# Performance work log

Measured on AMD Instinct MI355X. Metric: run time of the kernel, lower is better.

The kernel has to match this reference:

```python
import jax, jax.numpy as jnp
import numpy as np

NUM_THING = 80
THING_STUFF_IDS = np.concatenate([np.arange(80), np.arange(80, 133)])  # thing_class_ids + stuff_class_ids
H_OUT, W_OUT = 641, 641
PIXEL_CONF_THR = 0.4
CLASS_CONF_THR = 0.7
NEG = -1e9  # mask value standing in for removing undetected slots


def _resize_bilinear_align_corners(x, h_out, w_out):
    # x: [h_in, w_in, C]; tf.compat.v1.image.resize_bilinear(..., align_corners=True)
    h_in, w_in = x.shape[0], x.shape[1]
    ys = jnp.linspace(0.0, h_in - 1.0, h_out)
    xs = jnp.linspace(0.0, w_in - 1.0, w_out)
    y0 = jnp.floor(ys).astype(jnp.int32)
    x0 = jnp.floor(xs).astype(jnp.int32)
    y1 = jnp.minimum(y0 + 1, h_in - 1)
    x1 = jnp.minimum(x0 + 1, w_in - 1)
    wy = (ys - y0.astype(ys.dtype))[:, None, None]
    wx = (xs - x0.astype(xs.dtype))[None, :, None]
    rows = x[y0] * (1.0 - wy) + x[y1] * wy          # [h_out, w_in, C]
    return rows[:, x0] * (1.0 - wx) + rows[:, x1] * wx  # [h_out, w_out, C]


def setup_inputs() -> dict:
    key = jax.random.key(0)
    k1, k2 = jax.random.split(key)
    pixel_space_mask_logits = jax.random.normal(k1, (161, 161, 128), dtype=jnp.float32)
    transformer_class_probs = jax.random.uniform(k2, (128, 134), dtype=jnp.float32)
    return {"pixel_space_mask_logits": pixel_space_mask_logits,
            "transformer_class_probs": transformer_class_probs}


def reference(pixel_space_mask_logits, transformer_class_probs):
    # --- _get_transformer_class_prediction (void channel dropped first) ---
    probs = transformer_class_probs[:, :-1]                     # [M, C]
    cls_pred = jnp.argmax(probs, axis=-1).astype(jnp.float32)   # [M]
    cls_conf = jnp.max(probs, axis=-1)                          # [M]
    detected = cls_conf >= CLASS_CONF_THR                       # [M] bool
    num_detections = jnp.sum(detected.astype(jnp.int32))
    # index of each detected slot within the detected subset (matches tf.gather order)
    det_subset_index = jnp.cumsum(detected.astype(jnp.int32)) - 1  # [M]

    # --- resize logits to full image (pieces=1 -> single full-width piece) ---
    resized = _resize_bilinear_align_corners(pixel_space_mask_logits, H_OUT, W_OUT)  # [H, W, M]

    # mask out undetected slots instead of gathering (same math, static shape)
    masked = jnp.where(detected[None, None, :], resized, NEG)   # [H, W, M]

    full_max = jnp.max(resized, axis=-1)                        # [H, W]
    det_max = jnp.max(masked, axis=-1)                          # [H, W]
    detected_pixel = (full_max == det_max).astype(jnp.float32)

    pixel_conf = jnp.max(jax.nn.softmax(masked, axis=-1), axis=-1)
    confident_region = (pixel_conf > PIXEL_CONF_THR).astype(jnp.float32) * detected_pixel

    argmax_slot = jnp.argmax(masked, axis=-1)                   # [H, W] slot index
    mask_id_map = det_subset_index[argmax_slot]                 # index within detected subset
    sem_float = cls_pred[argmax_slot]                           # detected_mask_class_pred gathered

    thing_mask = (sem_float < NUM_THING).astype(jnp.float32) * confident_region
    stuff_mask = (sem_float >= NUM_THING).astype(jnp.float32) * confident_region
    semantic_map = jnp.asarray(THING_STUFF_IDS, jnp.int32)[jnp.round(sem_float).astype(jnp.int32)]
    mask_id_map_plus_one = mask_id_map.astype(jnp.int32) + 1

    # --- empty-detection branch (tf.cond) expressed as select ---
    has_det = num_detections > 0
    mask_id_map_plus_one = jnp.where(has_det, mask_id_map_plus_one, jnp.ones_like(mask_id_map_plus_one))
    semantic_map = jnp.where(has_det, semantic_map, jnp.zeros_like(semantic_map))
    thing_mask = jnp.where(has_det, thing_mask, jnp.zeros_like(thing_mask))
    stuff_mask = jnp.where(has_det, stuff_mask, jnp.zeros_like(stuff_mask))
    return (mask_id_map_plus_one, semantic_map, thing_mask, stuff_mask)
```

## Files before the change

### kernel.cpp

```cpp
#include <hip/hip_runtime.h>

#pragma clang fp contract(off)

#define NP 410881

__global__ __launch_bounds__(1024) void slot_kernel(
    const float* __restrict__ probs, float* __restrict__ cls_pred,
    int* __restrict__ det_idx, unsigned long long* __restrict__ det_mask,
    int* __restrict__ num_det) {
  __shared__ float s_val[128];
  __shared__ int s_arg[128];
  __shared__ int s_tot0;
  int tid = threadIdx.x;
  int wv = tid >> 6, lane = tid & 63;

  float bvv[8];
  int bii[8];
#pragma unroll
  for (int k = 0; k < 8; ++k) {
    int r = wv * 8 + k;
    const float* row = probs + r * 134;
    float v0 = row[lane];
    float v1 = row[lane + 64];
    float v2 = (lane < 5) ? row[lane + 128] : -1.0f;
    float bv = v0;
    int bi = lane;
    if (v1 > bv) { bv = v1; bi = lane + 64; }
    if (v2 > bv) { bv = v2; bi = lane + 128; }
    bvv[k] = bv; bii[k] = bi;
  }
#pragma unroll
  for (int k = 0; k < 8; ++k) {
    float bv = bvv[k];
    int bi = bii[k];
#pragma unroll
    for (int off = 32; off; off >>= 1) {
      float ov = __shfl_xor(bv, off);
      int oi = __shfl_xor(bi, off);
      if (ov > bv || (ov == bv && oi < bi)) { bv = ov; bi = oi; }
    }
    if (lane == 0) { s_val[wv * 8 + k] = bv; s_arg[wv * 8 + k] = bi; }
  }
  __syncthreads();

  bool flag = false;
  unsigned long long b = 0;
  if (tid < 128) flag = s_val[tid] >= 0.7f;
  if (wv < 2) b = __ballot(flag);
  if (tid < 128 && lane == 0) {
    det_mask[wv] = b;
    if (wv == 0) s_tot0 = __popcll(b);
  }
  __syncthreads();
  if (tid < 128) {
    int incl = __popcll(b & ((1ull << lane) - 1)) + (flag ? 1 : 0) +
               (wv ? s_tot0 : 0);
    det_idx[tid] = incl - 1;
    cls_pred[tid] = (float)s_arg[tid];
    if (tid == 127) *num_det = incl;
  }
}

__global__ __launch_bounds__(128) void post_kernel(
    const float* __restrict__ logits, const float* __restrict__ ws_cls,
    const int* __restrict__ ws_didx,
    const unsigned long long* __restrict__ ws_mask,
    const int* __restrict__ ws_ndet, float* __restrict__ out) {
#pragma clang fp contract(off)
  __shared__ float tex[25 * 132];
  __shared__ float s_cls[128];
  __shared__ int s_didx[128];
  int tid = threadIdx.x;
  int X0 = blockIdx.x << 4, Y0 = blockIdx.y << 4;

  int strip = tid & 7, py = tid >> 3;
  int cx = strip >> 1, h = strip & 1;
  int cy = py >> 2;
  int xa = X0 + (cx << 2) + (h << 1);
  int y = Y0 + py;

  int ndet = *ws_ndet;
  if (ndet == 0) {
    if (y < 641) {
      if (xa < 641) {
        int i0 = y * 641 + xa;
        out[i0] = 1.0f; out[NP + i0] = 0.f; out[2 * NP + i0] = 0.f; out[3 * NP + i0] = 0.f;
      }
      if (xa + 1 < 641) {
        int i1 = y * 641 + xa + 1;
        out[i1] = 1.0f; out[NP + i1] = 0.f; out[2 * NP + i1] = 0.f; out[3 * NP + i1] = 0.f;
      }
    }
    return;
  }

  int tX = blockIdx.x << 2, tY = blockIdx.y << 2;
  for (int f = tid; f < 800; f += 128) {
    int r = f / 160;
    int i = f - r * 160;
    int cc = i >> 5, c4 = i & 31;
    int gy = min(tY + r, 160);
    int gx = min(tX + cc, 160);
    float4 v = *(const float4*)(logits + ((gy * 161 + gx) << 7) + (c4 << 2));
    *(float4*)(tex + (r * 5 + cc) * 132 + (c4 << 2)) = v;
  }
  s_cls[tid] = ws_cls[tid];
  s_didx[tid] = ws_didx[tid];
  __syncthreads();

  const float* p0 = tex + (cy * 5 + cx) * 132;
  const float* p1 = p0 + 5 * 132;
  float wy = 0.25f * (float)(py & 3);
  float iwy = 1.0f - wy;
  float wx0 = 0.5f * (float)h;
  float wx1 = wx0 + 0.25f;
  float iwx0 = 1.0f - wx0, iwx1 = 1.0f - wx1;

  float m0 = -INFINITY, m1 = -INFINITY;
  int am0 = 0, am1 = 0;
  float T0 = 0.f, T1 = 0.f;
  bool dp0 = true, dp1 = true;

  if (ndet == 128) {
    float ms0[4], ms1[4], Ts0[4], Ts1[4];
    int as0[4], as1[4];
#pragma unroll
    for (int j = 0; j < 4; ++j) {
      ms0[j] = -INFINITY; ms1[j] = -INFINITY;
      Ts0[j] = 0.f; Ts1[j] = 0.f;
      as0[j] = 0; as1[j] = 0;
    }
#define CH(A00, A01, A10, A11, CIDX, J)                                        \
  {                                                                            \
    float r0 = (A00) * iwy + (A10) * wy;                                       \
    float r1 = (A01) * iwy + (A11) * wy;                                       \
    float v0 = r0 * iwx0 + r1 * wx0;                                           \
    float v1 = r0 * iwx1 + r1 * wx1;                                           \
    bool g0 = v0 > ms0[J]; ms0[J] = g0 ? v0 : ms0[J]; as0[J] = g0 ? (CIDX) : as0[J]; \
    bool g1 = v1 > ms1[J]; ms1[J] = g1 ? v1 : ms1[J]; as1[J] = g1 ? (CIDX) : as1[J]; \
    Ts0[J] += __expf(v0);                                                      \
    Ts1[J] += __expf(v1);                                                      \
  }
#pragma unroll 2
    for (int c = 0; c < 128; c += 4) {
      float4 q00 = *(const float4*)(p0 + c);
      float4 q01 = *(const float4*)(p0 + c + 132);
      float4 q10 = *(const float4*)(p1 + c);
      float4 q11 = *(const float4*)(p1 + c + 132);
      CH(q00.x, q01.x, q10.x, q11.x, c + 0, 0);
      CH(q00.y, q01.y, q10.y, q11.y, c + 1, 1);
      CH(q00.z, q01.z, q10.z, q11.z, c + 2, 2);
      CH(q00.w, q01.w, q10.w, q11.w, c + 3, 3);
    }
#undef CH
    m0 = ms0[0]; am0 = as0[0]; m1 = ms1[0]; am1 = as1[0];
#pragma unroll
    for (int j = 1; j < 4; ++j) {
      if (ms0[j] > m0 || (ms0[j] == m0 && as0[j] < am0)) { m0 = ms0[j]; am0 = as0[j]; }
      if (ms1[j] > m1 || (ms1[j] == m1 && as1[j] < am1)) { m1 = ms1[j]; am1 = as1[j]; }
    }
    T0 = (Ts0[0] + Ts0[1]) + (Ts0[2] + Ts0[3]);
    T1 = (Ts1[0] + Ts1[1]) + (Ts1[2] + Ts1[3]);
  } else {
    unsigned long long mlo = ws_mask[0], mhi = ws_mask[1];
    float rm0 = -INFINITY, rm1 = -INFINITY;
#pragma unroll 4
    for (int c = 0; c < 128; ++c) {
      float a00 = p0[c], a01 = p0[c + 132];
      float a10 = p1[c], a11 = p1[c + 132];
      float r0 = a00 * iwy + a10 * wy;
      float r1 = a01 * iwy + a11 * wy;
      float v0 = r0 * iwx0 + r1 * wx0;
      float v1 = r0 * iwx1 + r1 * wx1;
      rm0 = fmaxf(rm0, v0);
      rm1 = fmaxf(rm1, v1);
      unsigned long long bit = (c < 64) ? (mlo >> c) : (mhi >> (c - 64));
      if (bit & 1) {
        bool g0 = v0 > m0; m0 = g0 ? v0 : m0; am0 = g0 ? c : am0;
        bool g1 = v1 > m1; m1 = g1 ? v1 : m1; am1 = g1 ? c : am1;
        T0 += __expf(v0);
        T1 += __expf(v1);
      }
    }
    dp0 = (rm0 == m0);
    dp1 = (rm1 == m1);
  }

  float cg0 = ((__expf(m0) > 0.4f * T0) && dp0) ? 1.0f : 0.0f;
  float cg1 = ((__expf(m1) > 0.4f * T1) && dp1) ? 1.0f : 0.0f;
  float sem0 = s_cls[am0], sem1 = s_cls[am1];
  float mid0 = (float)(s_didx[am0] + 1), mid1 = (float)(s_didx[am1] + 1);
  float th0 = (sem0 < 80.f) ? cg0 : 0.f;
  float st0 = cg0 - th0;
  float th1 = (sem1 < 80.f) ? cg1 : 0.f;
  float st1 = cg1 - th1;

  if (y < 641) {
    if (xa < 641) {
      int i0 = y * 641 + xa;
      out[i0] = mid0; out[NP + i0] = sem0; out[2 * NP + i0] = th0; out[3 * NP + i0] = st0;
    }
    if (xa + 1 < 641) {
      int i1 = y * 641 + xa + 1;
      out[i1] = mid1; out[NP + i1] = sem1; out[2 * NP + i1] = th1; out[3 * NP + i1] = st1;
    }
  }
}

extern "C" void kernel_launch(void* const* d_in, const int* in_sizes, int n_in,
                              void* d_out, int out_size, void* d_ws,
                              size_t ws_size, hipStream_t stream) {
  const float* logits = (const float*)d_in[0];
  const float* probs = (const float*)d_in[1];
  float* out = (float*)d_out;

  float* ws_f = (float*)d_ws;
  float* cls_pred = ws_f;
  int* det_idx = (int*)(ws_f + 128);
  unsigned long long* det_mask = (unsigned long long*)(ws_f + 256);
  int* num_det = (int*)(ws_f + 260);

  slot_kernel<<<1, 1024, 0, stream>>>(probs, cls_pred, det_idx, det_mask,
                                      num_det);

  dim3 grid(41, 41);
  post_kernel<<<grid, 128, 0, stream>>>(logits, cls_pred, det_idx, det_mask,
                                        num_det, out);
}
```

Before: 95.00 us.

## Fuse slot classification into the per-tile kernel and drop workspace round-trip

Removes the single-block slot kernel and has every tile block recompute per-slot argmax and detection mask from the class probabilities, one slot per thread. Logit tile loads are issued into registers before that computation so their latency overlaps it. Detected-subset indices are derived with popcount over the ballot mask instead of a precomputed table. This saves one kernel launch and its dependency. In exchange, all 1681 blocks redundantly read the 128x134 probability matrix with a serial per-thread scan and use more registers for staging.

```diff
diff --git a/kernel.cpp b/kernel.cpp
--- a/kernel.cpp
+++ b/kernel.cpp
@@ -4,72 +4,13 @@
 
 #define NP 410881
 
-__global__ __launch_bounds__(1024) void slot_kernel(
-    const float* __restrict__ probs, float* __restrict__ cls_pred,
-    int* __restrict__ det_idx, unsigned long long* __restrict__ det_mask,
-    int* __restrict__ num_det) {
-  __shared__ float s_val[128];
-  __shared__ int s_arg[128];
-  __shared__ int s_tot0;
-  int tid = threadIdx.x;
-  int wv = tid >> 6, lane = tid & 63;
-
-  float bvv[8];
-  int bii[8];
-#pragma unroll
-  for (int k = 0; k < 8; ++k) {
-    int r = wv * 8 + k;
-    const float* row = probs + r * 134;
-    float v0 = row[lane];
-    float v1 = row[lane + 64];
-    float v2 = (lane < 5) ? row[lane + 128] : -1.0f;
-    float bv = v0;
-    int bi = lane;
-    if (v1 > bv) { bv = v1; bi = lane + 64; }
-    if (v2 > bv) { bv = v2; bi = lane + 128; }
-    bvv[k] = bv; bii[k] = bi;
-  }
-#pragma unroll
-  for (int k = 0; k < 8; ++k) {
-    float bv = bvv[k];
-    int bi = bii[k];
-#pragma unroll
-    for (int off = 32; off; off >>= 1) {
-      float ov = __shfl_xor(bv, off);
-      int oi = __shfl_xor(bi, off);
-      if (ov > bv || (ov == bv && oi < bi)) { bv = ov; bi = oi; }
-    }
-    if (lane == 0) { s_val[wv * 8 + k] = bv; s_arg[wv * 8 + k] = bi; }
-  }
-  __syncthreads();
-
-  bool flag = false;
-  unsigned long long b = 0;
-  if (tid < 128) flag = s_val[tid] >= 0.7f;
-  if (wv < 2) b = __ballot(flag);
-  if (tid < 128 && lane == 0) {
-    det_mask[wv] = b;
-    if (wv == 0) s_tot0 = __popcll(b);
-  }
-  __syncthreads();
-  if (tid < 128) {
-    int incl = __popcll(b & ((1ull << lane) - 1)) + (flag ? 1 : 0) +
-               (wv ? s_tot0 : 0);
-    det_idx[tid] = incl - 1;
-    cls_pred[tid] = (float)s_arg[tid];
-    if (tid == 127) *num_det = incl;
-  }
-}
-
-__global__ __launch_bounds__(128) void post_kernel(
-    const float* __restrict__ logits, const float* __restrict__ ws_cls,
-    const int* __restrict__ ws_didx,
-    const unsigned long long* __restrict__ ws_mask,
-    const int* __restrict__ ws_ndet, float* __restrict__ out) {
+__global__ __launch_bounds__(128) void fused_kernel(
+    const float* __restrict__ logits, const float* __restrict__ probs,
+    float* __restrict__ out) {
 #pragma clang fp contract(off)
   __shared__ float tex[25 * 132];
   __shared__ float s_cls[128];
-  __shared__ int s_didx[128];
+  __shared__ unsigned long long s_mask[2];
   int tid = threadIdx.x;
   int X0 = blockIdx.x << 4, Y0 = blockIdx.y << 4;
 
@@ -79,7 +20,57 @@
   int xa = X0 + (cx << 2) + (h << 1);
   int y = Y0 + py;
 
-  int ndet = *ws_ndet;
+  int tX = blockIdx.x << 2, tY = blockIdx.y << 2;
+  float4 stg[7];
+#pragma unroll
+  for (int k = 0; k < 7; ++k) {
+    int f = tid + (k << 7);
+    if (f < 800) {
+      int r = f / 160;
+      int i = f - r * 160;
+      int cc = i >> 5, c4 = i & 31;
+      int gy = min(tY + r, 160);
+      int gx = min(tX + cc, 160);
+      stg[k] = *(const float4*)(logits + ((gy * 161 + gx) << 7) + (c4 << 2));
+    }
+  }
+
+  {
+    const float2* row = (const float2*)(probs + tid * 134);
+    float mA = -INFINITY, mB = -INFINITY;
+    int aA = 0, aB = 1;
+#pragma unroll 4
+    for (int j = 0; j < 66; ++j) {
+      float2 v = row[j];
+      if (v.x > mA) { mA = v.x; aA = 2 * j; }
+      if (v.y > mB) { mB = v.y; aB = 2 * j + 1; }
+    }
+    float v132 = probs[tid * 134 + 132];
+    if (v132 > mA) { mA = v132; aA = 132; }
+    float bv = mA;
+    int bi = aA;
+    if (mB > bv || (mB == bv && aB < bi)) { bv = mB; bi = aB; }
+    s_cls[tid] = (float)bi;
+    bool det = bv >= 0.7f;
+    unsigned long long b = __ballot(det);
+    if ((tid & 63) == 0) s_mask[tid >> 6] = b;
+  }
+
+#pragma unroll
+  for (int k = 0; k < 7; ++k) {
+    int f = tid + (k << 7);
+    if (f < 800) {
+      int r = f / 160;
+      int i = f - r * 160;
+      int cc = i >> 5, c4 = i & 31;
+      *(float4*)(tex + (r * 5 + cc) * 132 + (c4 << 2)) = stg[k];
+    }
+  }
+  __syncthreads();
+
+  unsigned long long mlo = s_mask[0], mhi = s_mask[1];
+  int ndet = __popcll(mlo) + __popcll(mhi);
+
   if (ndet == 0) {
     if (y < 641) {
       if (xa < 641) {
@@ -94,20 +85,6 @@
     return;
   }
 
-  int tX = blockIdx.x << 2, tY = blockIdx.y << 2;
-  for (int f = tid; f < 800; f += 128) {
-    int r = f / 160;
-    int i = f - r * 160;
-    int cc = i >> 5, c4 = i & 31;
-    int gy = min(tY + r, 160);
-    int gx = min(tX + cc, 160);
-    float4 v = *(const float4*)(logits + ((gy * 161 + gx) << 7) + (c4 << 2));
-    *(float4*)(tex + (r * 5 + cc) * 132 + (c4 << 2)) = v;
-  }
-  s_cls[tid] = ws_cls[tid];
-  s_didx[tid] = ws_didx[tid];
-  __syncthreads();
-
   const float* p0 = tex + (cy * 5 + cx) * 132;
   const float* p1 = p0 + 5 * 132;
   float wy = 0.25f * (float)(py & 3);
@@ -162,7 +139,6 @@
     T0 = (Ts0[0] + Ts0[1]) + (Ts0[2] + Ts0[3]);
     T1 = (Ts1[0] + Ts1[1]) + (Ts1[2] + Ts1[3]);
   } else {
-    unsigned long long mlo = ws_mask[0], mhi = ws_mask[1];
     float rm0 = -INFINITY, rm1 = -INFINITY;
 #pragma unroll 4
     for (int c = 0; c < 128; ++c) {
@@ -189,7 +165,30 @@
   float cg0 = ((__expf(m0) > 0.4f * T0) && dp0) ? 1.0f : 0.0f;
   float cg1 = ((__expf(m1) > 0.4f * T1) && dp1) ? 1.0f : 0.0f;
   float sem0 = s_cls[am0], sem1 = s_cls[am1];
-  float mid0 = (float)(s_didx[am0] + 1), mid1 = (float)(s_didx[am1] + 1);
+
+  float mid0, mid1;
+  if (ndet == 128) {
+    mid0 = (float)(am0 + 1);
+    mid1 = (float)(am1 + 1);
+  } else {
+    int a = am0;
+    unsigned long long ml = (a >= 63) ? mlo : (mlo & ((1ull << (a + 1)) - 1));
+    int cnt = __popcll(ml);
+    if (a >= 64) {
+      unsigned long long mh = (a >= 127) ? mhi : (mhi & ((1ull << (a - 63)) - 1));
+      cnt += __popcll(mh);
+    }
+    mid0 = (float)cnt;
+    a = am1;
+    ml = (a >= 63) ? mlo : (mlo & ((1ull << (a + 1)) - 1));
+    cnt = __popcll(ml);
+    if (a >= 64) {
+      unsigned long long mh = (a >= 127) ? mhi : (mhi & ((1ull << (a - 63)) - 1));
+      cnt += __popcll(mh);
+    }
+    mid1 = (float)cnt;
+  }
+
   float th0 = (sem0 < 80.f) ? cg0 : 0.f;
   float st0 = cg0 - th0;
   float th1 = (sem1 < 80.f) ? cg1 : 0.f;
@@ -213,17 +212,8 @@
   const float* logits = (const float*)d_in[0];
   const float* probs = (const float*)d_in[1];
   float* out = (float*)d_out;
-
-  float* ws_f = (float*)d_ws;
-  float* cls_pred = ws_f;
-  int* det_idx = (int*)(ws_f + 128);
-  unsigned long long* det_mask = (unsigned long long*)(ws_f + 256);
-  int* num_det = (int*)(ws_f + 260);
-
-  slot_kernel<<<1, 1024, 0, stream>>>(probs, cls_pred, det_idx, det_mask,
-                                      num_det);
+  (void)d_ws; (void)ws_size;
 
   dim3 grid(41, 41);
-  post_kernel<<<grid, 128, 0, stream>>>(logits, cls_pred, det_idx, det_mask,
-                                        num_det, out);
+  fused_kernel<<<grid, 128, 0, stream>>>(logits, probs, out);
 }
```

Result: slower. 102.7 us (+8.1%).

## Split slot channels across two thread halves and widen output tiles

Applied to the files above, without the earlier changes.

Each block now covers a 32x16 output tile with 512 threads. Two halves of 256 threads each process 64 of the 128 slot channels for the same pixels, then merge max, argmax, exp-sum and raw-max through shared memory. The wider tile cuts redundant halo loads of the low-resolution logits, and the channel split halves the serial per-thread loop. The cost is a second barrier plus a reduction step, more shared memory per block, and only half the threads active during the final write phase.

```diff
diff --git a/kernel.cpp b/kernel.cpp
--- a/kernel.cpp
+++ b/kernel.cpp
@@ -61,19 +61,25 @@
   }
 }
 
-__global__ __launch_bounds__(128) void post_kernel(
+__global__ __launch_bounds__(512) void post_kernel(
     const float* __restrict__ logits, const float* __restrict__ ws_cls,
     const int* __restrict__ ws_didx,
     const unsigned long long* __restrict__ ws_mask,
     const int* __restrict__ ws_ndet, float* __restrict__ out) {
 #pragma clang fp contract(off)
-  __shared__ float tex[25 * 132];
+  __shared__ float tex[45 * 132];
   __shared__ float s_cls[128];
   __shared__ int s_didx[128];
+  __shared__ float s_pf[6 * 256];
+  __shared__ int s_pai[2 * 256];
+
   int tid = threadIdx.x;
-  int X0 = blockIdx.x << 4, Y0 = blockIdx.y << 4;
-
-  int strip = tid & 7, py = tid >> 3;
+  int lt = tid & 255;
+  int half = tid >> 8;
+  int cbase = half << 6;
+
+  int X0 = blockIdx.x << 5, Y0 = blockIdx.y << 4;
+  int strip = lt & 15, py = lt >> 4;
   int cx = strip >> 1, h = strip & 1;
   int cy = py >> 2;
   int xa = X0 + (cx << 2) + (h << 1);
@@ -81,7 +87,7 @@
 
   int ndet = *ws_ndet;
   if (ndet == 0) {
-    if (y < 641) {
+    if (half == 0 && y < 641) {
       if (xa < 641) {
         int i0 = y * 641 + xa;
         out[i0] = 1.0f; out[NP + i0] = 0.f; out[2 * NP + i0] = 0.f; out[3 * NP + i0] = 0.f;
@@ -94,22 +100,30 @@
     return;
   }
 
-  int tX = blockIdx.x << 2, tY = blockIdx.y << 2;
-  for (int f = tid; f < 800; f += 128) {
-    int r = f / 160;
-    int i = f - r * 160;
-    int cc = i >> 5, c4 = i & 31;
-    int gy = min(tY + r, 160);
-    int gx = min(tX + cc, 160);
-    float4 v = *(const float4*)(logits + ((gy * 161 + gx) << 7) + (c4 << 2));
-    *(float4*)(tex + (r * 5 + cc) * 132 + (c4 << 2)) = v;
-  }
-  s_cls[tid] = ws_cls[tid];
-  s_didx[tid] = ws_didx[tid];
-  __syncthreads();
-
-  const float* p0 = tex + (cy * 5 + cx) * 132;
-  const float* p1 = p0 + 5 * 132;
+  int tX = blockIdx.x << 3, tY = blockIdx.y << 2;
+#pragma unroll
+  for (int k = 0; k < 3; ++k) {
+    int f = tid + (k << 9);
+    if (f < 1440) {
+      int r = f / 288;
+      int i = f - r * 288;
+      int cc = i >> 5, c4 = i & 31;
+      int gy = min(tY + r, 160);
+      int gx = min(tX + cc, 160);
+      float4 v = *(const float4*)(logits + ((gy * 161 + gx) << 7) + (c4 << 2));
+      *(float4*)(tex + (r * 9 + cc) * 132 + (c4 << 2)) = v;
+    }
+  }
+  if (tid < 128) {
+    s_cls[tid] = ws_cls[tid];
+    s_didx[tid] = ws_didx[tid];
+  }
+  __syncthreads();
+
+  unsigned long long mlo = ws_mask[0], mhi = ws_mask[1];
+
+  const float* p0 = tex + (cy * 9 + cx) * 132 + cbase;
+  const float* p1 = p0 + 9 * 132;
   float wy = 0.25f * (float)(py & 3);
   float iwy = 1.0f - wy;
   float wx0 = 0.5f * (float)h;
@@ -117,9 +131,9 @@
   float iwx0 = 1.0f - wx0, iwx1 = 1.0f - wx1;
 
   float m0 = -INFINITY, m1 = -INFINITY;
-  int am0 = 0, am1 = 0;
+  int am0 = cbase, am1 = cbase;
   float T0 = 0.f, T1 = 0.f;
-  bool dp0 = true, dp1 = true;
+  float rm0 = -INFINITY, rm1 = -INFINITY;
 
   if (ndet == 128) {
     float ms0[4], ms1[4], Ts0[4], Ts1[4];
@@ -128,7 +142,7 @@
     for (int j = 0; j < 4; ++j) {
       ms0[j] = -INFINITY; ms1[j] = -INFINITY;
       Ts0[j] = 0.f; Ts1[j] = 0.f;
-      as0[j] = 0; as1[j] = 0;
+      as0[j] = cbase + j; as1[j] = cbase + j;
     }
 #define CH(A00, A01, A10, A11, CIDX, J)                                        \
   {                                                                            \
@@ -142,15 +156,15 @@
     Ts1[J] += __expf(v1);                                                      \
   }
 #pragma unroll 2
-    for (int c = 0; c < 128; c += 4) {
+    for (int c = 0; c < 64; c += 4) {
       float4 q00 = *(const float4*)(p0 + c);
       float4 q01 = *(const float4*)(p0 + c + 132);
       float4 q10 = *(const float4*)(p1 + c);
       float4 q11 = *(const float4*)(p1 + c + 132);
-      CH(q00.x, q01.x, q10.x, q11.x, c + 0, 0);
-      CH(q00.y, q01.y, q10.y, q11.y, c + 1, 1);
-      CH(q00.z, q01.z, q10.z, q11.z, c + 2, 2);
-      CH(q00.w, q01.w, q10.w, q11.w, c + 3, 3);
+      CH(q00.x, q01.x, q10.x, q11.x, cbase + c + 0, 0);
+      CH(q00.y, q01.y, q10.y, q11.y, cbase + c + 1, 1);
+      CH(q00.z, q01.z, q10.z, q11.z, cbase + c + 2, 2);
+      CH(q00.w, q01.w, q10.w, q11.w, cbase + c + 3, 3);
     }
 #undef CH
     m0 = ms0[0]; am0 = as0[0]; m1 = ms1[0]; am1 = as1[0];
@@ -161,11 +175,11 @@
     }
     T0 = (Ts0[0] + Ts0[1]) + (Ts0[2] + Ts0[3]);
     T1 = (Ts1[0] + Ts1[1]) + (Ts1[2] + Ts1[3]);
+    rm0 = m0; rm1 = m1;
   } else {
-    unsigned long long mlo = ws_mask[0], mhi = ws_mask[1];
-    float rm0 = -INFINITY, rm1 = -INFINITY;
+    unsigned long long mm = half ? mhi : mlo;
 #pragma unroll 4
-    for (int c = 0; c < 128; ++c) {
+    for (int c = 0; c < 64; ++c) {
       float a00 = p0[c], a01 = p0[c + 132];
       float a10 = p1[c], a11 = p1[c + 132];
       float r0 = a00 * iwy + a10 * wy;
@@ -174,17 +188,33 @@
       float v1 = r0 * iwx1 + r1 * wx1;
       rm0 = fmaxf(rm0, v0);
       rm1 = fmaxf(rm1, v1);
-      unsigned long long bit = (c < 64) ? (mlo >> c) : (mhi >> (c - 64));
-      if (bit & 1) {
-        bool g0 = v0 > m0; m0 = g0 ? v0 : m0; am0 = g0 ? c : am0;
-        bool g1 = v1 > m1; m1 = g1 ? v1 : m1; am1 = g1 ? c : am1;
+      if ((mm >> c) & 1) {
+        bool g0 = v0 > m0; m0 = g0 ? v0 : m0; am0 = g0 ? cbase + c : am0;
+        bool g1 = v1 > m1; m1 = g1 ? v1 : m1; am1 = g1 ? cbase + c : am1;
         T0 += __expf(v0);
         T1 += __expf(v1);
       }
     }
-    dp0 = (rm0 == m0);
-    dp1 = (rm1 == m1);
-  }
+  }
+
+  if (half) {
+    s_pf[0 * 256 + lt] = m0; s_pf[1 * 256 + lt] = T0; s_pf[2 * 256 + lt] = rm0;
+    s_pf[3 * 256 + lt] = m1; s_pf[4 * 256 + lt] = T1; s_pf[5 * 256 + lt] = rm1;
+    s_pai[lt] = am0; s_pai[256 + lt] = am1;
+  }
+  __syncthreads();
+  if (half) return;
+
+  {
+    float mh0 = s_pf[0 * 256 + lt], Th0 = s_pf[1 * 256 + lt], rh0 = s_pf[2 * 256 + lt];
+    float mh1 = s_pf[3 * 256 + lt], Th1 = s_pf[4 * 256 + lt], rh1 = s_pf[5 * 256 + lt];
+    int ah0 = s_pai[lt], ah1 = s_pai[256 + lt];
+    if (mh0 > m0) { m0 = mh0; am0 = ah0; }
+    if (mh1 > m1) { m1 = mh1; am1 = ah1; }
+    rm0 = fmaxf(rm0, rh0); rm1 = fmaxf(rm1, rh1);
+    T0 += Th0; T1 += Th1;
+  }
+  bool dp0 = (rm0 == m0), dp1 = (rm1 == m1);
 
   float cg0 = ((__expf(m0) > 0.4f * T0) && dp0) ? 1.0f : 0.0f;
   float cg1 = ((__expf(m1) > 0.4f * T1) && dp1) ? 1.0f : 0.0f;
@@ -223,7 +253,7 @@
   slot_kernel<<<1, 1024, 0, stream>>>(probs, cls_pred, det_idx, det_mask,
                                       num_det);
 
-  dim3 grid(41, 41);
-  post_kernel<<<grid, 128, 0, stream>>>(logits, cls_pred, det_idx, det_mask,
+  dim3 grid(21, 41);
+  post_kernel<<<grid, 512, 0, stream>>>(logits, cls_pred, det_idx, det_mask,
                                         num_det, out);
 }
```

Result: no change. 93.16 us (-1.9%).
